# Kernel optimization log

Measured on AMD Instinct MI355X. Metric: run time of the kernel, lower is better.

The kernel has to match this reference:

```python
import jax, jax.numpy as jnp
import numpy as np
import math

B, S, H = 2, 2048, 1024
NH, HD = 16, 64  # num heads, head dim; NH*HD == H


def setup_inputs() -> dict:
    key = jax.random.key(0)
    k1, k2, k3 = jax.random.split(key, 3)
    hidden_states = jax.random.normal(k1, (B, S, H), dtype=jnp.float32)
    # causal multiplicative mask [1,1,S,S], 1.0 where attending is allowed
    mask = jnp.tril(jnp.ones((S, S), dtype=jnp.float32))[None, None]
    W_qkv = jax.random.normal(k2, (H, 3 * H), dtype=jnp.float32) * (1.0 / math.sqrt(H))
    b_qkv = jnp.zeros((3 * H,), dtype=jnp.float32)
    W_out = jax.random.normal(k3, (H, H), dtype=jnp.float32) * (1.0 / math.sqrt(H))
    b_out = jnp.zeros((H,), dtype=jnp.float32)
    return {"hidden_states": hidden_states, "mask": mask, "W_qkv": W_qkv,
            "b_qkv": b_qkv, "W_out": W_out, "b_out": b_out}


def reference(hidden_states, mask, W_qkv, b_qkv, W_out, b_out):
    b, s, h = hidden_states.shape
    # fused QKV projection then split into contiguous thirds (split_tensor_along_last_dim)
    qkv = jnp.einsum('bsh,hd->bsd', hidden_states, W_qkv) + b_qkv
    q, k, v = jnp.split(qkv, 3, axis=-1)
    # [b, s, nh*hd] -> [b, nh, s, hd]
    def to_heads(t):
        return t.reshape(b, s, NH, HD).transpose(0, 2, 1, 3)
    q, k, v = to_heads(q), to_heads(k), to_heads(v)
    q = q / jnp.sqrt(jnp.float32(HD))  # scaling_attention_score=True
    scores = jnp.einsum('bhqd,bhkd->bhqk', q, k)  # [b,nh,s,s]
    # multiplicative mask + large-negative bias trick from standard_attention
    scores = scores * mask - 10000.0 * (1.0 - mask)
    probs = jax.nn.softmax(scores, axis=-1)
    ctx = jnp.einsum('bhqk,bhkd->bhqd', probs, v)
    ctx = ctx.transpose(0, 2, 1, 3).reshape(b, s, h)  # [b, s, nh*hd]
    return jnp.einsum('bsh,hd->bsd', ctx, W_out) + b_out
```

## Files before the change

kernel.cpp:

```cpp
#include <hip/hip_runtime.h>
#include <cstdint>
#include <cstddef>

#define NHEAD 16
#define HDIM 64
#define SEQ 2048
#define BATCH 2
#define HID 1024

typedef __bf16 bf16x8 __attribute__((ext_vector_type(8)));
typedef float f32x4 __attribute__((ext_vector_type(4)));

#define AS1 __attribute__((address_space(1)))
#define AS3 __attribute__((address_space(3)))

__device__ __forceinline__ unsigned short f2bf(float f) {
    union { float f; unsigned u; } v; v.f = f;
    unsigned r = v.u + 0x7fffu + ((v.u >> 16) & 1u);
    return (unsigned short)(r >> 16);
}

__device__ __forceinline__ unsigned cvtpk_bf16(float a, float b) {
    unsigned d;
    asm("v_cvt_pk_bf16_f32 %0, %1, %2" : "=v"(d) : "v"(a), "v"(b));
    return d;
}

__global__ __launch_bounds__(256) void convert_f32_bf16(
    const float* __restrict__ in, unsigned short* __restrict__ out, int n) {
    int i = (blockIdx.x * 256 + threadIdx.x) * 8;
    if (i >= n) return;
    float4 a = *(const float4*)(in + i);
    float4 b = *(const float4*)(in + i + 4);
    uint4 o;
    o.x = (unsigned)f2bf(a.x) | ((unsigned)f2bf(a.y) << 16);
    o.y = (unsigned)f2bf(a.z) | ((unsigned)f2bf(a.w) << 16);
    o.z = (unsigned)f2bf(b.x) | ((unsigned)f2bf(b.y) << 16);
    o.w = (unsigned)f2bf(b.z) | ((unsigned)f2bf(b.w) << 16);
    *(uint4*)(out + i) = o;
}

__global__ __launch_bounds__(256) void transpose_f32_bf16(
    const float* __restrict__ in, unsigned short* __restrict__ out, int R, int C) {
    __shared__ unsigned short T[64][72];
    int t = threadIdx.x;
    int c0 = blockIdx.x * 64, r0 = blockIdx.y * 64;
    for (int p = 0; p < 4; ++p) {
        int idx = (p * 256 + t) * 4;
        int row = idx >> 6, col = idx & 63;
        float4 v = *(const float4*)(in + (size_t)(r0 + row) * C + c0 + col);
        T[row][col + 0] = f2bf(v.x);
        T[row][col + 1] = f2bf(v.y);
        T[row][col + 2] = f2bf(v.z);
        T[row][col + 3] = f2bf(v.w);
    }
    __syncthreads();
    for (int p = 0; p < 4; ++p) {
        int idx = (p * 256 + t) * 4;
        int orow = idx >> 6, ocol = idx & 63;
        ushort4 u;
        u.x = T[ocol + 0][orow];
        u.y = T[ocol + 1][orow];
        u.z = T[ocol + 2][orow];
        u.w = T[ocol + 3][orow];
        *(ushort4*)(out + (size_t)(c0 + orow) * R + r0 + ocol) = u;
    }
}

__global__ __launch_bounds__(512, 2) void gemm_qkv(
    const unsigned short* __restrict__ A, const unsigned short* __restrict__ Bt,
    const float* __restrict__ bias,
    unsigned short* __restrict__ Qb, unsigned short* __restrict__ Kb,
    unsigned short* __restrict__ Vt) {
    __shared__ unsigned short LDSu[81920];
    const int NT = 16;
    int tid = threadIdx.x;
    int wave = tid >> 6, lane = tid & 63, ln = lane & 15, quad = lane >> 4;
    int wm = wave >> 2, wn = wave & 3;
    int fid = blockIdx.y * 12 + blockIdx.x;
    int xcd = fid & 7, jj0 = fid >> 3;
    int by = (xcd & 3) * 4 + jj0 / 6;
    int bx = (xcd >> 2) * 6 + jj0 % 6;
    int m0 = by * 256, n0 = bx * 256;

    int rsub = lane >> 3;
    int gs = (lane & 7) ^ rsub;

    auto stage = [&](int h) {
        if (h >= 4 * NT) return;
        int T = h >> 2, jj = h & 3;
        const unsigned short* src;
        int slot;
        if (jj < 2) {
            slot = (2 * T + jj) % 6;
            src = A + (size_t)(m0 + jj * 128) * 1024 + T * 64;
        } else {
            slot = 6 + (2 * T + (jj - 2)) % 4;
            src = Bt + (size_t)(n0 + (jj - 2) * 128) * 1024 + T * 64;
        }
#pragma unroll
        for (int p = 0; p < 2; ++p) {
            __builtin_amdgcn_global_load_lds(
                (const AS1 void*)(src + (size_t)(p * 64 + wave * 8 + rsub) * 1024 + gs * 8),
                (AS3 void*)&LDSu[slot * 8192 + (p * 8 + wave) * 512], 16, 0, 0);
        }
    };

    f32x4 zero4 = {0.f, 0.f, 0.f, 0.f};
    f32x4 acc[8][4];
#pragma unroll
    for (int i = 0; i < 8; ++i)
#pragma unroll
        for (int k = 0; k < 4; ++k) acc[i][k] = zero4;

    for (int h = 0; h < 6; ++h) stage(h);
    asm volatile("s_waitcnt vmcnt(4)" ::: "memory");
    __builtin_amdgcn_s_barrier();

    for (int t = 0; t < NT; ++t) {
        int myA = (2 * t + wm) % 6;
        int myB = 6 + (2 * t + (wn >> 1)) % 4;
        const unsigned short* as = &LDSu[myA * 8192];
        const unsigned short* bs = &LDSu[myB * 8192];
        int brow = (wn & 1) * 64;
        bf16x8 bfr[4][2];
#pragma unroll
        for (int j = 0; j < 4; ++j) {
            if (j == 0) {
#pragma unroll
                for (int fn = 0; fn < 4; ++fn)
#pragma unroll
                    for (int ks = 0; ks < 2; ++ks)
                        bfr[fn][ks] = *(const bf16x8*)
                            &bs[(brow + fn * 16 + ln) * 64 + (((ks * 4 + quad) ^ (ln & 7)) * 8)];
            }
            bf16x8 af[2][2];
#pragma unroll
            for (int mi = 0; mi < 2; ++mi)
#pragma unroll
                for (int ks = 0; ks < 2; ++ks)
                    af[mi][ks] = *(const bf16x8*)
                        &as[((2 * j + mi) * 16 + ln) * 64 + (((ks * 4 + quad) ^ (ln & 7)) * 8)];
            stage(4 * t + j + 6);
            if (j == 3 && t < NT - 1) {
                if (t == NT - 2) asm volatile("s_waitcnt vmcnt(0)" ::: "memory");
                else             asm volatile("s_waitcnt vmcnt(4)" ::: "memory");
            }
            __builtin_amdgcn_s_barrier();
            asm volatile("s_waitcnt lgkmcnt(0)" ::: "memory");
            __builtin_amdgcn_sched_barrier(0);
            __builtin_amdgcn_s_setprio(1);
#pragma unroll
            for (int mi = 0; mi < 2; ++mi)
#pragma unroll
                for (int fn = 0; fn < 4; ++fn) {
                    acc[2 * j + mi][fn] = __builtin_amdgcn_mfma_f32_16x16x32_bf16(
                        af[mi][0], bfr[fn][0], acc[2 * j + mi][fn], 0, 0, 0);
                    acc[2 * j + mi][fn] = __builtin_amdgcn_mfma_f32_16x16x32_bf16(
                        af[mi][1], bfr[fn][1], acc[2 * j + mi][fn], 0, 0, 0);
                }
            __builtin_amdgcn_s_setprio(0);
            __builtin_amdgcn_s_barrier();
        }
    }

    int nbase = n0 + wn * 64;
#pragma unroll
    for (int fn = 0; fn < 4; ++fn) {
        int gn = nbase + fn * 16 + ln;
        float bv = bias[gn];
        int third = gn >> 10;
        int rem = gn & 1023;
        int h = rem >> 6, d = rem & 63;
        if (third == 2) {
#pragma unroll
            for (int fm = 0; fm < 8; ++fm) {
                int gm = m0 + wm * 128 + fm * 16 + quad * 4;
                int b = gm >> 11, s = gm & 2047;
                size_t bh = (size_t)(b * NHEAD + h);
                ushort4 u;
                u.x = f2bf(acc[fm][fn][0] + bv);
                u.y = f2bf(acc[fm][fn][1] + bv);
                u.z = f2bf(acc[fm][fn][2] + bv);
                u.w = f2bf(acc[fm][fn][3] + bv);
                *(ushort4*)&Vt[(bh * HDIM + d) * SEQ + s] = u;
            }
        } else {
            unsigned short* dst = third == 0 ? Qb : Kb;
            float scale = third == 0 ? 0.1803368801111f : 1.0f;
#pragma unroll
            for (int fm = 0; fm < 8; ++fm) {
#pragma unroll
                for (int r = 0; r < 4; ++r) {
                    int gm = m0 + wm * 128 + fm * 16 + quad * 4 + r;
                    int b = gm >> 11, s = gm & 2047;
                    size_t bh = (size_t)(b * NHEAD + h);
                    dst[(bh * SEQ + s) * HDIM + d] = f2bf((acc[fm][fn][r] + bv) * scale);
                }
            }
        }
    }
}

__global__ __launch_bounds__(256) void gemm_out(
    const unsigned short* __restrict__ A, const unsigned short* __restrict__ Bt,
    const float* __restrict__ bias, float* __restrict__ C) {
    __shared__ unsigned short As[64][32];
    __shared__ unsigned short Bs[128][32];
    int t = threadIdx.x;
    int wave = t >> 6, lane = t & 63, ln = lane & 15, quad = lane >> 4;
    int wm = wave >> 1, wn = wave & 1;
    int fid = blockIdx.y * 8 + blockIdx.x;
    int xcd = fid & 7, jj = fid >> 3;
    int by = xcd * 8 + (jj >> 3);
    int bx = jj & 7;
    int m0 = by * 64, n0 = bx * 128;
    int srow = lane >> 2, scol = (lane & 3) * 8;
    f32x4 zero4 = {0.f, 0.f, 0.f, 0.f};
    f32x4 acc[2][4];
    for (int mi = 0; mi < 2; ++mi)
        for (int ni = 0; ni < 4; ++ni) acc[mi][ni] = zero4;
    for (int kt = 0; kt < 1024; kt += 32) {
        __builtin_amdgcn_global_load_lds(
            (const AS1 void*)(A + (size_t)(m0 + wave * 16 + srow) * 1024 + kt + scol),
            (AS3 void*)&As[wave * 16][0], 16, 0, 0);
        for (int p = 0; p < 2; ++p) {
            int r0 = (wave * 2 + p) * 16 + srow;
            __builtin_amdgcn_global_load_lds(
                (const AS1 void*)(Bt + (size_t)(n0 + r0) * 1024 + kt + scol),
                (AS3 void*)&Bs[(wave * 2 + p) * 16][0], 16, 0, 0);
        }
        __syncthreads();
        bf16x8 af[2], bfr[4];
        for (int mi = 0; mi < 2; ++mi)
            af[mi] = *(const bf16x8*)&As[wm * 32 + mi * 16 + ln][quad * 8];
        for (int ni = 0; ni < 4; ++ni)
            bfr[ni] = *(const bf16x8*)&Bs[wn * 64 + ni * 16 + ln][quad * 8];
        for (int mi = 0; mi < 2; ++mi)
            for (int ni = 0; ni < 4; ++ni)
                acc[mi][ni] = __builtin_amdgcn_mfma_f32_16x16x32_bf16(
                    af[mi], bfr[ni], acc[mi][ni], 0, 0, 0);
        __syncthreads();
    }
    int nbase = n0 + wn * 64;
    for (int ni = 0; ni < 4; ++ni) {
        int gn = nbase + ni * 16 + ln;
        float bv = bias[gn];
        for (int mi = 0; mi < 2; ++mi) {
            for (int r = 0; r < 4; ++r) {
                int gm = m0 + wm * 32 + mi * 16 + quad * 4 + r;
                C[(size_t)gm * HID + gn] = acc[mi][ni][r] + bv;
            }
        }
    }
}

__global__ __launch_bounds__(256, 2) void flash_attn(
    const unsigned short* __restrict__ Qb, const unsigned short* __restrict__ Kb,
    const unsigned short* __restrict__ Vt, unsigned short* __restrict__ Ctx) {
    __shared__ unsigned short KsB[3][64][64];
    __shared__ unsigned short VsB[3][64][64];
    __shared__ unsigned short Ps[2][4][16][72];
    int tid = threadIdx.x;
    int wave = tid >> 6, lane = tid & 63, ln = lane & 15, quad = lane >> 4;

    int id = blockIdx.y * 16 + blockIdx.x;
    int xcd = id & 7, j = id >> 3;
    int bh = xcd * 4 + (j & 3);
    int r0 = (j >> 2) & 7;
    int bxrole = (j < 32) ? r0 : 15 - r0;
    int qiA = bxrole;
    int qiB = 31 - bxrole;
    int q0A = qiA * 64, q0B = qiB * 64;
    const size_t baseQK = (size_t)bh * SEQ * HDIM;
    const size_t baseV = (size_t)bh * HDIM * SEQ;
    int b = bh >> 4, h = bh & 15;

    int rIn = lane >> 3;
    int gsw = ((lane & 7) ^ rIn) * 8;

    bf16x8 aqA0, aqA1, aqB0, aqB1;
    {
        const unsigned short* qp =
            Qb + baseQK + (size_t)(q0A + wave * 16 + ln) * HDIM + quad * 8;
        aqA0 = *(const bf16x8*)qp;
        aqA1 = *(const bf16x8*)(qp + 32);
        qp = Qb + baseQK + (size_t)(q0B + wave * 16 + ln) * HDIM + quad * 8;
        aqB0 = *(const bf16x8*)qp;
        aqB1 = *(const bf16x8*)(qp + 32);
    }

    auto prefetch = [&](int kj, int bi) {
        const unsigned short* kb = Kb + baseQK + (size_t)kj * 64 * HDIM;
        const unsigned short* vb = Vt + baseV + kj * 64;
        for (int c = wave; c < 8; c += 4) {
            __builtin_amdgcn_global_load_lds(
                (const AS1 void*)(kb + (c * 8 + rIn) * HDIM + gsw),
                (AS3 void*)&KsB[bi][c * 8][0], 16, 0, 0);
            __builtin_amdgcn_global_load_lds(
                (const AS1 void*)(vb + (size_t)(c * 8 + rIn) * SEQ + gsw),
                (AS3 void*)&VsB[bi][c * 8][0], 16, 0, 0);
        }
    };

    f32x4 zero4 = {0.f, 0.f, 0.f, 0.f};
    f32x4 oA[4], oB[4];
    float laccA = 0.f, laccB = 0.f;
    for (int i = 0; i < 4; ++i) { oA[i] = zero4; oB[i] = zero4; }

    auto epilogue = [&](const f32x4* o, float lacc, int q0) {
        float sum = lacc;
        sum += __shfl_xor(sum, 16);
        sum += __shfl_xor(sum, 32);
        float linv = __builtin_amdgcn_rcpf(sum);
        size_t rowb = ((size_t)(b * SEQ + q0 + wave * 16 + ln)) * HID + h * 64;
        for (int ni = 0; ni < 4; ++ni) {
            ushort4 u;
            u.x = f2bf(o[ni][0] * linv);
            u.y = f2bf(o[ni][1] * linv);
            u.z = f2bf(o[ni][2] * linv);
            u.w = f2bf(o[ni][3] * linv);
            *(ushort4*)&Ctx[rowb + ni * 16 + quad * 4] = u;
        }
    };

    prefetch(0, 0);
    prefetch(1, 1);
    for (int t = 0; t <= qiB; ++t) {
        if (t == qiB) asm volatile("s_waitcnt vmcnt(0)" ::: "memory");
        else          asm volatile("s_waitcnt vmcnt(4)" ::: "memory");
        __builtin_amdgcn_s_barrier();
        __builtin_amdgcn_sched_barrier(0);
        if (t + 2 <= qiB) prefetch(t + 2, (t + 2) % 3);
        int buf = t % 3;
        bool joint = (t <= qiA);

        bf16x8 akf[2][4];
#pragma unroll
        for (int kk = 0; kk < 2; ++kk)
#pragma unroll
            for (int ni = 0; ni < 4; ++ni)
                akf[kk][ni] = *(const bf16x8*)
                    &KsB[buf][ni * 16 + ln][((kk * 4 + quad) ^ (ln & 7)) * 8];
        f32x4 sA[4], sB[4];
#pragma unroll
        for (int ni = 0; ni < 4; ++ni) { sA[ni] = zero4; sB[ni] = zero4; }
        __builtin_amdgcn_s_setprio(1);
#pragma unroll
        for (int kk = 0; kk < 2; ++kk) {
            bf16x8 bq = kk ? aqB1 : aqB0;
#pragma unroll
            for (int ni = 0; ni < 4; ++ni)
                sB[ni] = __builtin_amdgcn_mfma_f32_16x16x32_bf16(akf[kk][ni], bq, sB[ni], 0, 0, 0);
        }
        if (joint) {
#pragma unroll
            for (int kk = 0; kk < 2; ++kk) {
                bf16x8 bq = kk ? aqA1 : aqA0;
#pragma unroll
                for (int ni = 0; ni < 4; ++ni)
                    sA[ni] = __builtin_amdgcn_mfma_f32_16x16x32_bf16(akf[kk][ni], bq, sA[ni], 0, 0, 0);
            }
        }
        __builtin_amdgcn_s_setprio(0);

        if (t == qiB) {
#pragma unroll
            for (int ni = 0; ni < 4; ++ni)
#pragma unroll
                for (int r = 0; r < 4; ++r)
                    if (ni * 16 + quad * 4 + r > wave * 16 + ln) sB[ni][r] = -1.0e38f;
        }
        if (t == qiA) {
#pragma unroll
            for (int ni = 0; ni < 4; ++ni)
#pragma unroll
                for (int r = 0; r < 4; ++r)
                    if (ni * 16 + quad * 4 + r > wave * 16 + ln) sA[ni][r] = -1.0e38f;
        }

#pragma unroll
        for (int ni = 0; ni < 4; ++ni) {
            float e0 = __builtin_amdgcn_exp2f(sB[ni][0]);
            float e1 = __builtin_amdgcn_exp2f(sB[ni][1]);
            float e2 = __builtin_amdgcn_exp2f(sB[ni][2]);
            float e3 = __builtin_amdgcn_exp2f(sB[ni][3]);
            laccB += (e0 + e1) + (e2 + e3);
            uint2 pw;
            pw.x = cvtpk_bf16(e0, e1);
            pw.y = cvtpk_bf16(e2, e3);
            *(uint2*)&Ps[0][wave][ln][ni * 16 + quad * 4] = pw;
        }
        if (joint) {
#pragma unroll
            for (int ni = 0; ni < 4; ++ni) {
                float e0 = __builtin_amdgcn_exp2f(sA[ni][0]);
                float e1 = __builtin_amdgcn_exp2f(sA[ni][1]);
                float e2 = __builtin_amdgcn_exp2f(sA[ni][2]);
                float e3 = __builtin_amdgcn_exp2f(sA[ni][3]);
                laccA += (e0 + e1) + (e2 + e3);
                uint2 pw;
                pw.x = cvtpk_bf16(e0, e1);
                pw.y = cvtpk_bf16(e2, e3);
                *(uint2*)&Ps[1][wave][ln][ni * 16 + quad * 4] = pw;
            }
        }

        bf16x8 avf[2][4];
#pragma unroll
        for (int kk = 0; kk < 2; ++kk)
#pragma unroll
            for (int ni = 0; ni < 4; ++ni)
                avf[kk][ni] = *(const bf16x8*)
                    &VsB[buf][ni * 16 + ln][((kk * 4 + quad) ^ (ln & 7)) * 8];
        {
            bf16x8 bp0 = *(const bf16x8*)&Ps[0][wave][ln][quad * 8];
            bf16x8 bp1 = *(const bf16x8*)&Ps[0][wave][ln][32 + quad * 8];
            __builtin_amdgcn_s_setprio(1);
#pragma unroll
            for (int ni = 0; ni < 4; ++ni)
                oB[ni] = __builtin_amdgcn_mfma_f32_16x16x32_bf16(avf[0][ni], bp0, oB[ni], 0, 0, 0);
#pragma unroll
            for (int ni = 0; ni < 4; ++ni)
                oB[ni] = __builtin_amdgcn_mfma_f32_16x16x32_bf16(avf[1][ni], bp1, oB[ni], 0, 0, 0);
            __builtin_amdgcn_s_setprio(0);
        }
        if (joint) {
            bf16x8 bp0 = *(const bf16x8*)&Ps[1][wave][ln][quad * 8];
            bf16x8 bp1 = *(const bf16x8*)&Ps[1][wave][ln][32 + quad * 8];
            __builtin_amdgcn_s_setprio(1);
#pragma unroll
            for (int ni = 0; ni < 4; ++ni)
                oA[ni] = __builtin_amdgcn_mfma_f32_16x16x32_bf16(avf[0][ni], bp0, oA[ni], 0, 0, 0);
#pragma unroll
            for (int ni = 0; ni < 4; ++ni)
                oA[ni] = __builtin_amdgcn_mfma_f32_16x16x32_bf16(avf[1][ni], bp1, oA[ni], 0, 0, 0);
            __builtin_amdgcn_s_setprio(0);
        }

        if (t == qiA) epilogue(oA, laccA, q0A);
        if (t == qiB) epilogue(oB, laccB, q0B);
    }
}

extern "C" void kernel_launch(void* const* d_in, const int* in_sizes, int n_in,
                              void* d_out, int out_size, void* d_ws, size_t ws_size,
                              hipStream_t stream) {
    const float* X = (const float*)d_in[0];
    const float* Wqkv = (const float*)d_in[2];
    const float* bqkv = (const float*)d_in[3];
    const float* Wout = (const float*)d_in[4];
    const float* bout = (const float*)d_in[5];
    float* out = (float*)d_out;

    char* ws = (char*)d_ws;
    unsigned short* Xb   = (unsigned short*)(ws + 0);
    unsigned short* W1t  = (unsigned short*)(ws + 8388608);
    unsigned short* W2t  = (unsigned short*)(ws + 14680064);
    unsigned short* Qb   = (unsigned short*)(ws + 16777216);
    unsigned short* Kb   = (unsigned short*)(ws + 25165824);
    unsigned short* Vt   = (unsigned short*)(ws + 33554432);
    unsigned short* Ctx  = (unsigned short*)(ws + 41943040);

    convert_f32_bf16<<<2048, 256, 0, stream>>>(X, Xb, 4194304);
    transpose_f32_bf16<<<dim3(48, 16), 256, 0, stream>>>(Wqkv, W1t, 1024, 3072);
    transpose_f32_bf16<<<dim3(16, 16), 256, 0, stream>>>(Wout, W2t, 1024, 1024);
    gemm_qkv<<<dim3(12, 16), 512, 0, stream>>>(Xb, W1t, bqkv, Qb, Kb, Vt);
    flash_attn<<<dim3(16, 32), 256, 0, stream>>>(Qb, Kb, Vt, Ctx);
    gemm_out<<<dim3(8, 64), 256, 0, stream>>>(Ctx, W2t, bout, out);
}
```

Before: 194.4 us.

## Split paired causal q-tiles into one q-tile per block with double buffering

Flash attention previously gave each block two complementary query tiles (A and B) that shared K/V loads, with a triple-buffered K/V ring. Now each block handles a single 64-row query tile, the grid doubles to 1024 blocks, the longest tiles are scheduled first, and K/V staging drops to two buffers with a plain __syncthreads per step. The smaller LDS and register footprint raise the launch bound to 3 blocks per CU. In exchange, K/V tiles are no longer shared between two query tiles, so global and LDS traffic roughly doubles, and the prefetch is only one tile ahead.

```diff
diff --git a/kernel.cpp b/kernel.cpp
--- a/kernel.cpp
+++ b/kernel.cpp
@@ -255,23 +255,20 @@
     }
 }
 
-__global__ __launch_bounds__(256, 2) void flash_attn(
+__global__ __launch_bounds__(256, 3) void flash_attn(
     const unsigned short* __restrict__ Qb, const unsigned short* __restrict__ Kb,
     const unsigned short* __restrict__ Vt, unsigned short* __restrict__ Ctx) {
-    __shared__ unsigned short KsB[3][64][64];
-    __shared__ unsigned short VsB[3][64][64];
-    __shared__ unsigned short Ps[2][4][16][72];
+    __shared__ unsigned short KsB[2][64][64];
+    __shared__ unsigned short VsB[2][64][64];
+    __shared__ unsigned short Ps[4][16][72];
     int tid = threadIdx.x;
     int wave = tid >> 6, lane = tid & 63, ln = lane & 15, quad = lane >> 4;
 
-    int id = blockIdx.y * 16 + blockIdx.x;
+    int id = blockIdx.y * 32 + blockIdx.x;
     int xcd = id & 7, j = id >> 3;
     int bh = xcd * 4 + (j & 3);
-    int r0 = (j >> 2) & 7;
-    int bxrole = (j < 32) ? r0 : 15 - r0;
-    int qiA = bxrole;
-    int qiB = 31 - bxrole;
-    int q0A = qiA * 64, q0B = qiB * 64;
+    int qi = 31 - (j >> 2);
+    int q0 = qi * 64;
     const size_t baseQK = (size_t)bh * SEQ * HDIM;
     const size_t baseV = (size_t)bh * HDIM * SEQ;
     int b = bh >> 4, h = bh & 15;
@@ -279,15 +276,12 @@
     int rIn = lane >> 3;
     int gsw = ((lane & 7) ^ rIn) * 8;
 
-    bf16x8 aqA0, aqA1, aqB0, aqB1;
+    bf16x8 aq0, aq1;
     {
         const unsigned short* qp =
-            Qb + baseQK + (size_t)(q0A + wave * 16 + ln) * HDIM + quad * 8;
-        aqA0 = *(const bf16x8*)qp;
-        aqA1 = *(const bf16x8*)(qp + 32);
-        qp = Qb + baseQK + (size_t)(q0B + wave * 16 + ln) * HDIM + quad * 8;
-        aqB0 = *(const bf16x8*)qp;
-        aqB1 = *(const bf16x8*)(qp + 32);
+            Qb + baseQK + (size_t)(q0 + wave * 16 + ln) * HDIM + quad * 8;
+        aq0 = *(const bf16x8*)qp;
+        aq1 = *(const bf16x8*)(qp + 32);
     }
 
     auto prefetch = [&](int kj, int bi) {
@@ -304,36 +298,15 @@
     };
 
     f32x4 zero4 = {0.f, 0.f, 0.f, 0.f};
-    f32x4 oA[4], oB[4];
-    float laccA = 0.f, laccB = 0.f;
-    for (int i = 0; i < 4; ++i) { oA[i] = zero4; oB[i] = zero4; }
-
-    auto epilogue = [&](const f32x4* o, float lacc, int q0) {
-        float sum = lacc;
-        sum += __shfl_xor(sum, 16);
-        sum += __shfl_xor(sum, 32);
-        float linv = __builtin_amdgcn_rcpf(sum);
-        size_t rowb = ((size_t)(b * SEQ + q0 + wave * 16 + ln)) * HID + h * 64;
-        for (int ni = 0; ni < 4; ++ni) {
-            ushort4 u;
-            u.x = f2bf(o[ni][0] * linv);
-            u.y = f2bf(o[ni][1] * linv);
-            u.z = f2bf(o[ni][2] * linv);
-            u.w = f2bf(o[ni][3] * linv);
-            *(ushort4*)&Ctx[rowb + ni * 16 + quad * 4] = u;
-        }
-    };
+    f32x4 o[4];
+    float lacc = 0.f;
+    for (int i = 0; i < 4; ++i) o[i] = zero4;
 
     prefetch(0, 0);
-    prefetch(1, 1);
-    for (int t = 0; t <= qiB; ++t) {
-        if (t == qiB) asm volatile("s_waitcnt vmcnt(0)" ::: "memory");
-        else          asm volatile("s_waitcnt vmcnt(4)" ::: "memory");
-        __builtin_amdgcn_s_barrier();
-        __builtin_amdgcn_sched_barrier(0);
-        if (t + 2 <= qiB) prefetch(t + 2, (t + 2) % 3);
-        int buf = t % 3;
-        bool joint = (t <= qiA);
+    for (int t = 0; t <= qi; ++t) {
+        __syncthreads();
+        if (t < qi) prefetch(t + 1, (t + 1) & 1);
+        int buf = t & 1;
 
         bf16x8 akf[2][4];
 #pragma unroll
@@ -342,68 +315,38 @@
             for (int ni = 0; ni < 4; ++ni)
                 akf[kk][ni] = *(const bf16x8*)
                     &KsB[buf][ni * 16 + ln][((kk * 4 + quad) ^ (ln & 7)) * 8];
-        f32x4 sA[4], sB[4];
-#pragma unroll
-        for (int ni = 0; ni < 4; ++ni) { sA[ni] = zero4; sB[ni] = zero4; }
+        f32x4 s4[4];
+#pragma unroll
+        for (int ni = 0; ni < 4; ++ni) s4[ni] = zero4;
         __builtin_amdgcn_s_setprio(1);
 #pragma unroll
         for (int kk = 0; kk < 2; ++kk) {
-            bf16x8 bq = kk ? aqB1 : aqB0;
+            bf16x8 bq = kk ? aq1 : aq0;
 #pragma unroll
             for (int ni = 0; ni < 4; ++ni)
-                sB[ni] = __builtin_amdgcn_mfma_f32_16x16x32_bf16(akf[kk][ni], bq, sB[ni], 0, 0, 0);
-        }
-        if (joint) {
-#pragma unroll
-            for (int kk = 0; kk < 2; ++kk) {
-                bf16x8 bq = kk ? aqA1 : aqA0;
-#pragma unroll
-                for (int ni = 0; ni < 4; ++ni)
-                    sA[ni] = __builtin_amdgcn_mfma_f32_16x16x32_bf16(akf[kk][ni], bq, sA[ni], 0, 0, 0);
-            }
+                s4[ni] = __builtin_amdgcn_mfma_f32_16x16x32_bf16(akf[kk][ni], bq, s4[ni], 0, 0, 0);
         }
         __builtin_amdgcn_s_setprio(0);
 
-        if (t == qiB) {
+        if (t == qi) {
 #pragma unroll
             for (int ni = 0; ni < 4; ++ni)
 #pragma unroll
                 for (int r = 0; r < 4; ++r)
-                    if (ni * 16 + quad * 4 + r > wave * 16 + ln) sB[ni][r] = -1.0e38f;
-        }
-        if (t == qiA) {
-#pragma unroll
-            for (int ni = 0; ni < 4; ++ni)
-#pragma unroll
-                for (int r = 0; r < 4; ++r)
-                    if (ni * 16 + quad * 4 + r > wave * 16 + ln) sA[ni][r] = -1.0e38f;
+                    if (ni * 16 + quad * 4 + r > wave * 16 + ln) s4[ni][r] = -1.0e38f;
         }
 
 #pragma unroll
         for (int ni = 0; ni < 4; ++ni) {
-            float e0 = __builtin_amdgcn_exp2f(sB[ni][0]);
-            float e1 = __builtin_amdgcn_exp2f(sB[ni][1]);
-            float e2 = __builtin_amdgcn_exp2f(sB[ni][2]);
-            float e3 = __builtin_amdgcn_exp2f(sB[ni][3]);
-            laccB += (e0 + e1) + (e2 + e3);
+            float e0 = __builtin_amdgcn_exp2f(s4[ni][0]);
+            float e1 = __builtin_amdgcn_exp2f(s4[ni][1]);
+            float e2 = __builtin_amdgcn_exp2f(s4[ni][2]);
+            float e3 = __builtin_amdgcn_exp2f(s4[ni][3]);
+            lacc += (e0 + e1) + (e2 + e3);
             uint2 pw;
             pw.x = cvtpk_bf16(e0, e1);
             pw.y = cvtpk_bf16(e2, e3);
-            *(uint2*)&Ps[0][wave][ln][ni * 16 + quad * 4] = pw;
-        }
-        if (joint) {
-#pragma unroll
-            for (int ni = 0; ni < 4; ++ni) {
-                float e0 = __builtin_amdgcn_exp2f(sA[ni][0]);
-                float e1 = __builtin_amdgcn_exp2f(sA[ni][1]);
-                float e2 = __builtin_amdgcn_exp2f(sA[ni][2]);
-                float e3 = __builtin_amdgcn_exp2f(sA[ni][3]);
-                laccA += (e0 + e1) + (e2 + e3);
-                uint2 pw;
-                pw.x = cvtpk_bf16(e0, e1);
-                pw.y = cvtpk_bf16(e2, e3);
-                *(uint2*)&Ps[1][wave][ln][ni * 16 + quad * 4] = pw;
-            }
+            *(uint2*)&Ps[wave][ln][ni * 16 + quad * 4] = pw;
         }
 
         bf16x8 avf[2][4];
@@ -413,33 +356,31 @@
             for (int ni = 0; ni < 4; ++ni)
                 avf[kk][ni] = *(const bf16x8*)
                     &VsB[buf][ni * 16 + ln][((kk * 4 + quad) ^ (ln & 7)) * 8];
-        {
-            bf16x8 bp0 = *(const bf16x8*)&Ps[0][wave][ln][quad * 8];
-            bf16x8 bp1 = *(const bf16x8*)&Ps[0][wave][ln][32 + quad * 8];
-            __builtin_amdgcn_s_setprio(1);
-#pragma unroll
-            for (int ni = 0; ni < 4; ++ni)
-                oB[ni] = __builtin_amdgcn_mfma_f32_16x16x32_bf16(avf[0][ni], bp0, oB[ni], 0, 0, 0);
-#pragma unroll
-            for (int ni = 0; ni < 4; ++ni)
-                oB[ni] = __builtin_amdgcn_mfma_f32_16x16x32_bf16(avf[1][ni], bp1, oB[ni], 0, 0, 0);
-            __builtin_amdgcn_s_setprio(0);
-        }
-        if (joint) {
-            bf16x8 bp0 = *(const bf16x8*)&Ps[1][wave][ln][quad * 8];
-            bf16x8 bp1 = *(const bf16x8*)&Ps[1][wave][ln][32 + quad * 8];
-            __builtin_amdgcn_s_setprio(1);
-#pragma unroll
-            for (int ni = 0; ni < 4; ++ni)
-                oA[ni] = __builtin_amdgcn_mfma_f32_16x16x32_bf16(avf[0][ni], bp0, oA[ni], 0, 0, 0);
-#pragma unroll
-            for (int ni = 0; ni < 4; ++ni)
-                oA[ni] = __builtin_amdgcn_mfma_f32_16x16x32_bf16(avf[1][ni], bp1, oA[ni], 0, 0, 0);
-            __builtin_amdgcn_s_setprio(0);
-        }
-
-        if (t == qiA) epilogue(oA, laccA, q0A);
-        if (t == qiB) epilogue(oB, laccB, q0B);
+        bf16x8 bp0 = *(const bf16x8*)&Ps[wave][ln][quad * 8];
+        bf16x8 bp1 = *(const bf16x8*)&Ps[wave][ln][32 + quad * 8];
+        __builtin_amdgcn_s_setprio(1);
+#pragma unroll
+        for (int ni = 0; ni < 4; ++ni)
+            o[ni] = __builtin_amdgcn_mfma_f32_16x16x32_bf16(avf[0][ni], bp0, o[ni], 0, 0, 0);
+#pragma unroll
+        for (int ni = 0; ni < 4; ++ni)
+            o[ni] = __builtin_amdgcn_mfma_f32_16x16x32_bf16(avf[1][ni], bp1, o[ni], 0, 0, 0);
+        __builtin_amdgcn_s_setprio(0);
+    }
+
+    float sum = lacc;
+    sum += __shfl_xor(sum, 16);
+    sum += __shfl_xor(sum, 32);
+    float linv = __builtin_amdgcn_rcpf(sum);
+    size_t rowb = ((size_t)(b * SEQ + q0 + wave * 16 + ln)) * HID + h * 64;
+#pragma unroll
+    for (int ni = 0; ni < 4; ++ni) {
+        ushort4 u;
+        u.x = f2bf(o[ni][0] * linv);
+        u.y = f2bf(o[ni][1] * linv);
+        u.z = f2bf(o[ni][2] * linv);
+        u.w = f2bf(o[ni][3] * linv);
+        *(ushort4*)&Ctx[rowb + ni * 16 + quad * 4] = u;
     }
 }
 
@@ -466,6 +407,6 @@
     transpose_f32_bf16<<<dim3(48, 16), 256, 0, stream>>>(Wqkv, W1t, 1024, 3072);
     transpose_f32_bf16<<<dim3(16, 16), 256, 0, stream>>>(Wout, W2t, 1024, 1024);
     gemm_qkv<<<dim3(12, 16), 512, 0, stream>>>(Xb, W1t, bqkv, Qb, Kb, Vt);
-    flash_attn<<<dim3(16, 32), 256, 0, stream>>>(Qb, Kb, Vt, Ctx);
+    flash_attn<<<dim3(32, 32), 256, 0, stream>>>(Qb, Kb, Vt, Ctx);
     gemm_out<<<dim3(8, 64), 256, 0, stream>>>(Ctx, W2t, bout, out);
 }
```

Result: faster. 186.1 us (-4.3%).
